# Kernel tuning notes

Hardware: AMD Instinct MI355X
Metric: run time of the kernel (lower is better)

Reference implementation:

```python
import jax, jax.numpy as jnp
import numpy as np

N_NODES = 100000
N_EDGES = 1600000
IN_CH = 128
OUT_CH = 64
NEG_SLOPE = 0.2
EPS = 1e-16


def setup_inputs() -> dict:
    key = jax.random.key(0)
    k1, k2, k3, k4 = jax.random.split(key, 4)
    x = jax.random.normal(k1, (N_NODES, IN_CH), dtype=jnp.float32)
    # torch Linear weight layout: [out, in], xavier-ish scale
    W = jax.random.normal(k2, (OUT_CH, IN_CH), dtype=jnp.float32) * (1.0 / np.sqrt(IN_CH))
    att = jax.random.normal(k3, (1, 2 * OUT_CH), dtype=jnp.float32) * 0.1
    edge_index = jax.random.randint(k4, (2, N_EDGES), 0, N_NODES, dtype=jnp.int64)
    return {"x": x, "W": W, "att": att, "edge_index": edge_index}


def reference(x, W, att, edge_index):
    # h = linear(x), no bias
    h = x @ W.T                      # [N, out]
    row, col = edge_index[0], edge_index[1]
    # (cat([h[row], h[col]]) * att).sum(-1) == (h @ att_src)[row] + (h @ att_dst)[col]
    att_src = att[0, :OUT_CH]
    att_dst = att[0, OUT_CH:]
    s_src = h @ att_src              # [N]
    s_dst = h @ att_dst              # [N]
    e = s_src[row] + s_dst[col]      # [E]
    alpha = jnp.exp(jax.nn.leaky_relu(e, negative_slope=NEG_SLOPE))
    denom = jax.ops.segment_sum(alpha, col, num_segments=N_NODES)   # [N]
    alpha = alpha / (denom[col] + EPS)                              # [E]
    msg = alpha[:, None] * h[row]                                   # [E, out]
    out = jax.ops.segment_sum(msg, col, num_segments=N_NODES)      # [N, out]
    return out
```

## Files before the change

### kernel.cpp

```cpp
#include <hip/hip_runtime.h>

#define N_NODES 100000
#define N_EDGES 1600000
#define IN_CH 128
#define OUT_CH 64
#define NEG_SLOPE 0.2f
#define EPS 1e-16f

#define B_SHIFT 10
#define NB 98
#define CAP 17408
#define EPB 2048
#define NBLK_BIN 782

__global__ __launch_bounds__(256) void k_proj(
    const float* __restrict__ x, const float* __restrict__ W,
    const float* __restrict__ att,
    float* __restrict__ h, float* __restrict__ ssrc, float* __restrict__ sdst)
{
    __shared__ float xbuf[4][IN_CH];
    const int lane = threadIdx.x & 63;
    const int wid  = __builtin_amdgcn_readfirstlane(threadIdx.x >> 6);

    float w[IN_CH];
#pragma unroll
    for (int k = 0; k < IN_CH; k += 4) {
        const float4 v = *reinterpret_cast<const float4*>(W + lane * IN_CH + k);
        w[k] = v.x; w[k + 1] = v.y; w[k + 2] = v.z; w[k + 3] = v.w;
    }
    const float a_src = att[lane];
    const float a_dst = att[OUT_CH + lane];

    const int gw = blockIdx.x * 4 + wid;
    const int nw = gridDim.x * 4;
    for (int n = gw; n < N_NODES; n += nw) {
        const float2 xv =
            *reinterpret_cast<const float2*>(x + (size_t)n * IN_CH + lane * 2);
        xbuf[wid][lane * 2]     = xv.x;
        xbuf[wid][lane * 2 + 1] = xv.y;
        asm volatile("s_waitcnt lgkmcnt(0)" ::: "memory");

        float acc0 = 0.f, acc1 = 0.f, acc2 = 0.f, acc3 = 0.f;
#pragma unroll
        for (int k = 0; k < IN_CH; k += 4) {
            const float4 xq = *reinterpret_cast<const float4*>(&xbuf[wid][k]);
            acc0 = fmaf(xq.x, w[k],     acc0);
            acc1 = fmaf(xq.y, w[k + 1], acc1);
            acc2 = fmaf(xq.z, w[k + 2], acc2);
            acc3 = fmaf(xq.w, w[k + 3], acc3);
        }
        const float acc = (acc0 + acc1) + (acc2 + acc3);
        h[(size_t)n * OUT_CH + lane] = acc;

        float rs = acc * a_src;
        float rd = acc * a_dst;
#pragma unroll
        for (int off = 32; off >= 1; off >>= 1) {
            rs += __shfl_xor(rs, off);
            rd += __shfl_xor(rd, off);
        }
        if (lane == 0) { ssrc[n] = rs; sdst[n] = rd; }
    }
}

__global__ __launch_bounds__(256) void k_bin(
    const int* __restrict__ ei, int* __restrict__ gcnt,
    int* __restrict__ gbuckets)
{
    __shared__ int hist[NB], base[NB], offs[NB];
    const int t = threadIdx.x;
    for (int i = t; i < NB; i += 256) hist[i] = 0;
    __syncthreads();

    const int e0 = blockIdx.x * EPB;
#pragma unroll
    for (int i = 0; i < 2; ++i) {
        const int e = e0 + (i * 256 + t) * 4;
        if (e + 4 <= N_EDGES) {
            const int4 c4 = *reinterpret_cast<const int4*>(ei + N_EDGES + e);
            atomicAdd(hist + (c4.x >> B_SHIFT), 1);
            atomicAdd(hist + (c4.y >> B_SHIFT), 1);
            atomicAdd(hist + (c4.z >> B_SHIFT), 1);
            atomicAdd(hist + (c4.w >> B_SHIFT), 1);
        }
    }
    __syncthreads();

    for (int i = t; i < NB; i += 256) {
        base[i] = atomicAdd(gcnt + i, hist[i]);
        offs[i] = 0;
    }
    __syncthreads();

#pragma unroll
    for (int i = 0; i < 2; ++i) {
        const int e = e0 + (i * 256 + t) * 4;
        if (e + 4 <= N_EDGES) {
            const int4 c4 = *reinterpret_cast<const int4*>(ei + N_EDGES + e);
            const int4 r4 = *reinterpret_cast<const int4*>(ei + e);
            int b, p;
            b = c4.x >> B_SHIFT; p = base[b] + atomicAdd(offs + b, 1);
            if (p < CAP) gbuckets[b * CAP + p] = (r4.x << B_SHIFT) | (c4.x & 1023);
            b = c4.y >> B_SHIFT; p = base[b] + atomicAdd(offs + b, 1);
            if (p < CAP) gbuckets[b * CAP + p] = (r4.y << B_SHIFT) | (c4.y & 1023);
            b = c4.z >> B_SHIFT; p = base[b] + atomicAdd(offs + b, 1);
            if (p < CAP) gbuckets[b * CAP + p] = (r4.z << B_SHIFT) | (c4.z & 1023);
            b = c4.w >> B_SHIFT; p = base[b] + atomicAdd(offs + b, 1);
            if (p < CAP) gbuckets[b * CAP + p] = (r4.w << B_SHIFT) | (c4.w & 1023);
        }
    }
}

__global__ __launch_bounds__(128) void k_scanb(
    const int* __restrict__ gcnt, int* __restrict__ bstart)
{
    __shared__ int lds[128];
    const int t = threadIdx.x;
    const int v = (t < NB) ? gcnt[t] : 0;
    lds[t] = v;
    __syncthreads();
    for (int off = 1; off < 128; off <<= 1) {
        const int add = (t >= off) ? lds[t - off] : 0;
        __syncthreads();
        lds[t] += add;
        __syncthreads();
    }
    if (t < NB) bstart[t] = lds[t] - v;
}

__global__ __launch_bounds__(1024) void k_csr(
    const int* __restrict__ gbuckets, const int* __restrict__ gcnt,
    const int* __restrict__ bstart,
    int* __restrict__ offsets, int* __restrict__ srow)
{
    __shared__ int counts[1024];
    __shared__ int scan[1024];
    const int t = threadIdx.x;
    const int b = blockIdx.x;
    int cnt = gcnt[b]; if (cnt > CAP) cnt = CAP;
    const int bs = bstart[b];
    const int* __restrict__ bucket = gbuckets + (size_t)b * CAP;

    counts[t] = 0;
    __syncthreads();
    for (int j = t; j < cnt; j += 1024)
        atomicAdd(counts + (bucket[j] & 1023), 1);
    __syncthreads();

    const int c = counts[t];
    scan[t] = c;
    __syncthreads();
    for (int off = 1; off < 1024; off <<= 1) {
        const int add = (t >= off) ? scan[t - off] : 0;
        __syncthreads();
        scan[t] += add;
        __syncthreads();
    }
    const int excl = scan[t] - c;
    offsets[b * 1024 + t] = bs + excl;
    counts[t] = excl;
    __syncthreads();

    for (int j = t; j < cnt; j += 1024) {
        const int p = bucket[j];
        const int pos = bs + atomicAdd(counts + (p & 1023), 1);
        srow[pos] = p >> B_SHIFT;
    }
}

__global__ __launch_bounds__(256) void k_gather(
    const int* __restrict__ srow, const int* __restrict__ offsets,
    const float* __restrict__ h,
    const float* __restrict__ ssrc, const float* __restrict__ sdst,
    float* __restrict__ out)
{
    const int lane = threadIdx.x & 63;
    const int c = blockIdx.x * 4 + (threadIdx.x >> 6);
    if (c >= N_NODES) return;

    const int start = __builtin_amdgcn_readfirstlane(offsets[c]);
    const int end   = __builtin_amdgcn_readfirstlane(offsets[c + 1]);
    const float sd = sdst[c];

    float acc0 = 0.f, acc1 = 0.f, acc2 = 0.f, acc3 = 0.f;
    float den0 = 0.f, den1 = 0.f, den2 = 0.f, den3 = 0.f;

    int j = start;
    const int end4 = start + ((end - start) & ~3);
    for (; j < end4; j += 4) {
        const int r0 = __builtin_amdgcn_readfirstlane(srow[j + 0]);
        const int r1 = __builtin_amdgcn_readfirstlane(srow[j + 1]);
        const int r2 = __builtin_amdgcn_readfirstlane(srow[j + 2]);
        const int r3 = __builtin_amdgcn_readfirstlane(srow[j + 3]);

        const float h0 = h[(size_t)r0 * OUT_CH + lane];
        const float h1 = h[(size_t)r1 * OUT_CH + lane];
        const float h2 = h[(size_t)r2 * OUT_CH + lane];
        const float h3 = h[(size_t)r3 * OUT_CH + lane];

        const float s0 = ssrc[r0] + sd;
        const float s1 = ssrc[r1] + sd;
        const float s2 = ssrc[r2] + sd;
        const float s3 = ssrc[r3] + sd;
        const float a0 = __expf(s0 > 0.f ? s0 : s0 * NEG_SLOPE);
        const float a1 = __expf(s1 > 0.f ? s1 : s1 * NEG_SLOPE);
        const float a2 = __expf(s2 > 0.f ? s2 : s2 * NEG_SLOPE);
        const float a3 = __expf(s3 > 0.f ? s3 : s3 * NEG_SLOPE);

        acc0 = fmaf(a0, h0, acc0); den0 += a0;
        acc1 = fmaf(a1, h1, acc1); den1 += a1;
        acc2 = fmaf(a2, h2, acc2); den2 += a2;
        acc3 = fmaf(a3, h3, acc3); den3 += a3;
    }
    for (; j < end; ++j) {
        const int r = __builtin_amdgcn_readfirstlane(srow[j]);
        const float hv = h[(size_t)r * OUT_CH + lane];
        const float s = ssrc[r] + sd;
        const float a = __expf(s > 0.f ? s : s * NEG_SLOPE);
        acc0 = fmaf(a, hv, acc0); den0 += a;
    }

    const float acc = (acc0 + acc1) + (acc2 + acc3);
    const float den = (den0 + den1) + (den2 + den3);
    out[(size_t)c * OUT_CH + lane] = acc / (den + EPS);
}

extern "C" void kernel_launch(void* const* d_in, const int* in_sizes, int n_in,
                              void* d_out, int out_size, void* d_ws, size_t ws_size,
                              hipStream_t stream) {
    const float* x   = (const float*)d_in[0];
    const float* W   = (const float*)d_in[1];
    const float* att = (const float*)d_in[2];
    const int*   ei  = (const int*)d_in[3];
    float* out = (float*)d_out;

    char* ws = (char*)d_ws;
    size_t off = 0;
    auto carve = [&](size_t bytes) {
        void* p = ws + off;
        off += (bytes + 255) & ~(size_t)255;
        return p;
    };
    float* h        = (float*)carve((size_t)N_NODES * OUT_CH * 4);
    float* ssrc     = (float*)carve(N_NODES * 4);
    float* sdst     = (float*)carve(N_NODES * 4);
    int*   gbuckets = (int*)carve((size_t)NB * CAP * 4);
    int*   gcnt     = (int*)carve(NB * 4);
    int*   bstart   = (int*)carve(NB * 4);
    int*   offsets  = (int*)carve((NB * 1024 + 4) * 4);
    int*   srow     = (int*)carve((size_t)N_EDGES * 4);

    hipMemsetAsync(gcnt, 0, NB * sizeof(int), stream);

    k_proj<<<2048, 256, 0, stream>>>(x, W, att, h, ssrc, sdst);
    k_bin<<<NBLK_BIN, 256, 0, stream>>>(ei, gcnt, gbuckets);
    k_scanb<<<1, 128, 0, stream>>>(gcnt, bstart);
    k_csr<<<NB, 1024, 0, stream>>>(gbuckets, gcnt, bstart, offsets, srow);
    k_gather<<<(N_NODES + 3) / 4, 256, 0, stream>>>(srow, offsets,
                                                    h, ssrc, sdst, out);
}
```

Before: 273.7 us.

## Rewrite projection as shared-memory tiled GEMM with 4x4 register blocking

Replaces the per-wave, per-node projection (W held in 128 registers per lane, one node at a time) with a block-tiled GEMM. Each block stages 64 nodes of x and a transposed W in LDS, and each thread computes a 4x4 output micro-tile. A small new kernel transposes W into a scratch buffer each call. The aim is to cut register pressure and raise arithmetic intensity through operand reuse, at the cost of one extra kernel launch, about 64KB of LDS per block, and possible LDS bank conflicts.

```diff
diff --git a/kernel.cpp b/kernel.cpp
--- a/kernel.cpp
+++ b/kernel.cpp
@@ -13,53 +13,105 @@
 #define EPB 2048
 #define NBLK_BIN 782
 
+#define PROJ_TILE 64
+#define NBLK_PROJ 1563
+
+__global__ __launch_bounds__(256) void k_wt(
+    const float* __restrict__ W, float* __restrict__ Wt)
+{
+    const int tid = blockIdx.x * 256 + threadIdx.x;
+    if (tid < OUT_CH * IN_CH) {
+        const int c = tid >> 7;
+        const int k = tid & (IN_CH - 1);
+        Wt[k * OUT_CH + c] = W[tid];
+    }
+}
+
 __global__ __launch_bounds__(256) void k_proj(
-    const float* __restrict__ x, const float* __restrict__ W,
+    const float* __restrict__ x, const float* __restrict__ Wt,
     const float* __restrict__ att,
     float* __restrict__ h, float* __restrict__ ssrc, float* __restrict__ sdst)
 {
-    __shared__ float xbuf[4][IN_CH];
-    const int lane = threadIdx.x & 63;
-    const int wid  = __builtin_amdgcn_readfirstlane(threadIdx.x >> 6);
-
-    float w[IN_CH];
-#pragma unroll
-    for (int k = 0; k < IN_CH; k += 4) {
-        const float4 v = *reinterpret_cast<const float4*>(W + lane * IN_CH + k);
-        w[k] = v.x; w[k + 1] = v.y; w[k + 2] = v.z; w[k + 3] = v.w;
-    }
-    const float a_src = att[lane];
-    const float a_dst = att[OUT_CH + lane];
-
-    const int gw = blockIdx.x * 4 + wid;
-    const int nw = gridDim.x * 4;
-    for (int n = gw; n < N_NODES; n += nw) {
-        const float2 xv =
-            *reinterpret_cast<const float2*>(x + (size_t)n * IN_CH + lane * 2);
-        xbuf[wid][lane * 2]     = xv.x;
-        xbuf[wid][lane * 2 + 1] = xv.y;
-        asm volatile("s_waitcnt lgkmcnt(0)" ::: "memory");
-
-        float acc0 = 0.f, acc1 = 0.f, acc2 = 0.f, acc3 = 0.f;
-#pragma unroll
-        for (int k = 0; k < IN_CH; k += 4) {
-            const float4 xq = *reinterpret_cast<const float4*>(&xbuf[wid][k]);
-            acc0 = fmaf(xq.x, w[k],     acc0);
-            acc1 = fmaf(xq.y, w[k + 1], acc1);
-            acc2 = fmaf(xq.z, w[k + 2], acc2);
-            acc3 = fmaf(xq.w, w[k + 3], acc3);
+    __shared__ float xs[PROJ_TILE][IN_CH];
+    __shared__ float ws[IN_CH][OUT_CH];
+    const int t = threadIdx.x;
+    const int gbase = blockIdx.x * PROJ_TILE;
+
+#pragma unroll
+    for (int i = 0; i < 8; ++i) {
+        const int f4 = i * 256 + t;
+        const int k  = f4 >> 4;
+        const int c0 = (f4 & 15) * 4;
+        *reinterpret_cast<float4*>(&ws[k][c0]) =
+            *reinterpret_cast<const float4*>(Wt + k * OUT_CH + c0);
+    }
+#pragma unroll
+    for (int i = 0; i < 8; ++i) {
+        const int f4 = i * 256 + t;
+        const int n  = f4 >> 5;
+        const int k0 = (f4 & 31) * 4;
+        float4 v = make_float4(0.f, 0.f, 0.f, 0.f);
+        if (gbase + n < N_NODES)
+            v = *reinterpret_cast<const float4*>(
+                    x + (size_t)(gbase + n) * IN_CH + k0);
+        *reinterpret_cast<float4*>(&xs[n][k0]) = v;
+    }
+    __syncthreads();
+
+    const int cg = t & 15;
+    const int ng = t >> 4;
+    const int c0 = cg * 4;
+
+    float acc[4][4];
+#pragma unroll
+    for (int i = 0; i < 4; ++i)
+#pragma unroll
+        for (int j = 0; j < 4; ++j) acc[i][j] = 0.f;
+
+#pragma unroll
+    for (int k4 = 0; k4 < IN_CH / 4; ++k4) {
+        float4 xr[4], wr[4];
+#pragma unroll
+        for (int i = 0; i < 4; ++i)
+            xr[i] = *reinterpret_cast<const float4*>(&xs[ng * 4 + i][k4 * 4]);
+#pragma unroll
+        for (int j = 0; j < 4; ++j)
+            wr[j] = *reinterpret_cast<const float4*>(&ws[k4 * 4 + j][c0]);
+#pragma unroll
+        for (int i = 0; i < 4; ++i) {
+#pragma unroll
+            for (int j = 0; j < 4; ++j) {
+                const float xe = j == 0 ? xr[i].x : j == 1 ? xr[i].y
+                               : j == 2 ? xr[i].z : xr[i].w;
+                acc[i][0] = fmaf(xe, wr[j].x, acc[i][0]);
+                acc[i][1] = fmaf(xe, wr[j].y, acc[i][1]);
+                acc[i][2] = fmaf(xe, wr[j].z, acc[i][2]);
+                acc[i][3] = fmaf(xe, wr[j].w, acc[i][3]);
+            }
         }
-        const float acc = (acc0 + acc1) + (acc2 + acc3);
-        h[(size_t)n * OUT_CH + lane] = acc;
-
-        float rs = acc * a_src;
-        float rd = acc * a_dst;
-#pragma unroll
-        for (int off = 32; off >= 1; off >>= 1) {
-            rs += __shfl_xor(rs, off);
-            rd += __shfl_xor(rd, off);
+    }
+
+    const float as0 = att[c0],          as1 = att[c0 + 1];
+    const float as2 = att[c0 + 2],      as3 = att[c0 + 3];
+    const float ad0 = att[OUT_CH + c0],     ad1 = att[OUT_CH + c0 + 1];
+    const float ad2 = att[OUT_CH + c0 + 2], ad3 = att[OUT_CH + c0 + 3];
+
+#pragma unroll
+    for (int i = 0; i < 4; ++i) {
+        const int n = gbase + ng * 4 + i;
+        if (n < N_NODES) {
+            *reinterpret_cast<float4*>(h + (size_t)n * OUT_CH + c0) =
+                make_float4(acc[i][0], acc[i][1], acc[i][2], acc[i][3]);
         }
-        if (lane == 0) { ssrc[n] = rs; sdst[n] = rd; }
+        float ps = acc[i][0] * as0 + acc[i][1] * as1
+                 + acc[i][2] * as2 + acc[i][3] * as3;
+        float pd = acc[i][0] * ad0 + acc[i][1] * ad1
+                 + acc[i][2] * ad2 + acc[i][3] * ad3;
+        ps += __shfl_xor(ps, 1); pd += __shfl_xor(pd, 1);
+        ps += __shfl_xor(ps, 2); pd += __shfl_xor(pd, 2);
+        ps += __shfl_xor(ps, 4); pd += __shfl_xor(pd, 4);
+        ps += __shfl_xor(ps, 8); pd += __shfl_xor(pd, 8);
+        if (cg == 0 && n < N_NODES) { ssrc[n] = ps; sdst[n] = pd; }
     }
 }
 
@@ -244,6 +296,7 @@
     float* h        = (float*)carve((size_t)N_NODES * OUT_CH * 4);
     float* ssrc     = (float*)carve(N_NODES * 4);
     float* sdst     = (float*)carve(N_NODES * 4);
+    float* Wt       = (float*)carve((size_t)IN_CH * OUT_CH * 4);
     int*   gbuckets = (int*)carve((size_t)NB * CAP * 4);
     int*   gcnt     = (int*)carve(NB * 4);
     int*   bstart   = (int*)carve(NB * 4);
@@ -252,7 +305,8 @@
 
     hipMemsetAsync(gcnt, 0, NB * sizeof(int), stream);
 
-    k_proj<<<2048, 256, 0, stream>>>(x, W, att, h, ssrc, sdst);
+    k_wt<<<(OUT_CH * IN_CH + 255) / 256, 256, 0, stream>>>(W, Wt);
+    k_proj<<<NBLK_PROJ, 256, 0, stream>>>(x, Wt, att, h, ssrc, sdst);
     k_bin<<<NBLK_BIN, 256, 0, stream>>>(ei, gcnt, gbuckets);
     k_scanb<<<1, 128, 0, stream>>>(gcnt, bstart);
     k_csr<<<NB, 1024, 0, stream>>>(gbuckets, gcnt, bstart, offsets, srow);
```

Result: slower. 658.0 us (+140.5%).
